# Kernel tuning notes

Measured on AMD Instinct MI355X. Metric: run time of the kernel, lower is better.

## Reference

```python
import jax, jax.numpy as jnp
import numpy as np

B, T, D = 4, 4096, 512
K = 8192  # codebook_size


def setup_inputs() -> dict:
    key = jax.random.key(0)
    k1, k2 = jax.random.split(key)
    x = jax.random.normal(k1, (B, T, D), dtype=jnp.float32)
    embed = jax.random.normal(k2, (K, D), dtype=jnp.float32)
    return {"x": x, "embed": embed}


def reference(x, embed):
    # preprocess: flatten all leading dims -> [N, D]
    shape = x.shape
    xf = x.reshape(-1, shape[-1])  # [N, D]
    # quantize: negative squared euclidean distance, argmax over codebook
    x_sq = jnp.sum(xf * xf, axis=1, keepdims=True)          # [N, 1]
    e_sq = jnp.sum(embed * embed, axis=1)[None, :]          # [1, K]
    dist = -(x_sq - 2.0 * (xf @ embed.T) + e_sq)            # [N, K]
    embed_ind = jnp.argmax(dist, axis=-1)                   # [N]
    embed_ind = embed_ind.reshape(shape[:-1])               # [B, T]
    quantize = embed[embed_ind]                             # [B, T, D]
    return (quantize, embed_ind)
```

## Files before the change

### kernel.cpp

```cpp
#include <hip/hip_runtime.h>
#include <cstddef>
#include <cstdint>

typedef unsigned short ushort_t;
typedef unsigned long long ull_t;
typedef __attribute__((ext_vector_type(8))) short short8;
typedef __attribute__((ext_vector_type(4))) float f32x4;

constexpr int D_ = 512, K_ = 8192, N_ = 16384;
constexpr float MARGIN = 0.75f;

__device__ __forceinline__ ushort_t f2bf(float f) {
  unsigned u = __float_as_uint(f);
  return (ushort_t)((u + 0x7FFFu + ((u >> 16) & 1u)) >> 16);
}
__device__ __forceinline__ unsigned flipf(float s) {
  unsigned u = __float_as_uint(s);
  return (u & 0x80000000u) ? ~u : (u | 0x80000000u);
}
__device__ __forceinline__ float unflipf(unsigned m) {
  unsigned u = (m & 0x80000000u) ? (m ^ 0x80000000u) : ~m;
  return __uint_as_float(u);
}
__device__ __forceinline__ ull_t umax64(ull_t a, ull_t b) { return a > b ? a : b; }
__device__ __forceinline__ ull_t umin64(ull_t a, ull_t b) { return a < b ? a : b; }

__device__ __forceinline__ void gld16(void* l, const void* g) {
  __builtin_amdgcn_global_load_lds((const __attribute__((address_space(1))) void*)g,
                                   (__attribute__((address_space(3))) void*)l, 16, 0, 0);
}

__global__ __launch_bounds__(256) void conv_all(const float* __restrict__ x,
                                                const float* __restrict__ e,
                                                char* __restrict__ xbt, char* __restrict__ ebt,
                                                float* __restrict__ ehs) {
  const int g = threadIdx.x & 15, rr = threadIdx.x >> 4;
  if ((int)blockIdx.x < 1024) {
    const int tile = blockIdx.x >> 3, rg = blockIdx.x & 7;
    const int r = rg * 16 + rr;
    const float4* src = (const float4*)(x + ((size_t)(tile * 128 + r)) * D_ + g * 32);
    float4 f[8];
#pragma unroll
    for (int q = 0; q < 8; ++q) f[q] = src[q];
    char* dbase = xbt + (size_t)tile * 131072 + g * 8192 + r * 16;
#pragma unroll
    for (int kq = 0; kq < 4; ++kq) {
      float4 a = f[kq * 2], b = f[kq * 2 + 1];
      short8 v;
      v[0] = (short)f2bf(a.x); v[1] = (short)f2bf(a.y); v[2] = (short)f2bf(a.z); v[3] = (short)f2bf(a.w);
      v[4] = (short)f2bf(b.x); v[5] = (short)f2bf(b.y); v[6] = (short)f2bf(b.z); v[7] = (short)f2bf(b.w);
      *(short8*)(dbase + kq * 2048) = v;
    }
  } else {
    const int bid = blockIdx.x - 1024;
    const int tile = bid >> 3, rg = bid & 7;
    const int r = rg * 16 + rr;
    const int col = tile * 128 + r;
    const float4* src = (const float4*)(e + (size_t)col * D_ + g * 32);
    float4 f[8];
    float ss = 0.f;
#pragma unroll
    for (int q = 0; q < 8; ++q) {
      f[q] = src[q];
      ss += f[q].x * f[q].x + f[q].y * f[q].y + f[q].z * f[q].z + f[q].w * f[q].w;
    }
    char* dbase = ebt + (size_t)tile * 131072 + g * 8192 + r * 16;
#pragma unroll
    for (int kq = 0; kq < 4; ++kq) {
      float4 a = f[kq * 2], b = f[kq * 2 + 1];
      short8 v;
      v[0] = (short)f2bf(a.x); v[1] = (short)f2bf(a.y); v[2] = (short)f2bf(a.z); v[3] = (short)f2bf(a.w);
      v[4] = (short)f2bf(b.x); v[5] = (short)f2bf(b.y); v[6] = (short)f2bf(b.z); v[7] = (short)f2bf(b.w);
      *(short8*)(dbase + kq * 2048) = v;
    }
#pragma unroll
    for (int m = 1; m < 16; m <<= 1) ss += __shfl_xor(ss, m);
    if (g == 0) ehs[col] = 0.5f * ss;
  }
}

__global__ __launch_bounds__(256, 4) void dist_mfma(const char* __restrict__ xbt,
                                                    const char* __restrict__ ebt,
                                                    const float* __restrict__ ehs,
                                                    ull_t* __restrict__ ppu,
                                                    float* __restrict__ pps2) {
  __shared__ alignas(16) char lds[32768];
  const int tid = threadIdx.x, w = tid >> 6, l = tid & 63;
  const int fid = blockIdx.x + blockIdx.y * 128;
  const int k8 = fid & 7, j = fid >> 3;
  const int by = k8 * 8 + (j & 7), bx = j >> 3;
  const int row0 = bx * 128, col0 = by * 128;
  const int wr = w >> 1, wc = w & 1;
  const char* xsrc = xbt + (size_t)bx * 131072;
  const char* esrc = ebt + (size_t)by * 131072;

#pragma unroll
  for (int i = 0; i < 2; ++i) {
    gld16(lds + w * 2048 + i * 1024, xsrc + w * 2048 + i * 1024 + l * 16);
    gld16(lds + 8192 + w * 2048 + i * 1024, esrc + w * 2048 + i * 1024 + l * 16);
  }
  __syncthreads();

  f32x4 acc[4][4] = {};
  for (int g = 0; g < 16; ++g) {
    char* cbase = lds + (g & 1) * 16384;
    if (g < 15) {
      char* nbase = lds + ((g + 1) & 1) * 16384;
#pragma unroll
      for (int i = 0; i < 2; ++i) {
        gld16(nbase + w * 2048 + i * 1024, xsrc + (g + 1) * 8192 + w * 2048 + i * 1024 + l * 16);
        gld16(nbase + 8192 + w * 2048 + i * 1024, esrc + (g + 1) * 8192 + w * 2048 + i * 1024 + l * 16);
      }
    }
    short8 a[4], b[4];
#pragma unroll
    for (int i = 0; i < 4; ++i)
      a[i] = *(const short8*)(cbase + (l >> 4) * 2048 + (wr * 64 + i * 16 + (l & 15)) * 16);
#pragma unroll
    for (int jj = 0; jj < 4; ++jj)
      b[jj] = *(const short8*)(cbase + 8192 + (l >> 4) * 2048 + (wc * 64 + jj * 16 + (l & 15)) * 16);
#pragma unroll
    for (int i = 0; i < 4; ++i)
#pragma unroll
      for (int jj = 0; jj < 4; ++jj)
        acc[i][jj] = __builtin_amdgcn_mfma_f32_16x16x32_bf16(a[i], b[jj], acc[i][jj], 0, 0, 0);
    __syncthreads();
  }

  float eh[4];
  unsigned ic[4];
#pragma unroll
  for (int jj = 0; jj < 4; ++jj) {
    int col = col0 + wc * 64 + jj * 16 + (l & 15);
    eh[jj] = ehs[col];
    ic[jj] = 0xFFFFFFFFu - (unsigned)col;
  }
#pragma unroll
  for (int i = 0; i < 4; ++i)
#pragma unroll
    for (int jj = 0; jj < 4; ++jj)
#pragma unroll
      for (int r = 0; r < 4; ++r)
        acc[i][jj][r] -= eh[jj];

  float mx[4][4];
#pragma unroll
  for (int i = 0; i < 4; ++i)
#pragma unroll
    for (int r = 0; r < 4; ++r)
      mx[i][r] = fmaxf(fmaxf(acc[i][0][r], acc[i][1][r]), fmaxf(acc[i][2][r], acc[i][3][r]));
#pragma unroll
  for (int m = 1; m < 16; m <<= 1)
#pragma unroll
    for (int i = 0; i < 4; ++i)
#pragma unroll
      for (int r = 0; r < 4; ++r)
        mx[i][r] = fmaxf(mx[i][r], __shfl_xor(mx[i][r], m));

  unsigned ii[4][4];
#pragma unroll
  for (int i = 0; i < 4; ++i)
#pragma unroll
    for (int r = 0; r < 4; ++r) {
      unsigned t0 = (acc[i][0][r] == mx[i][r]) ? ic[0] : 0u;
      unsigned t1 = (acc[i][1][r] == mx[i][r]) ? ic[1] : 0u;
      unsigned t2 = (acc[i][2][r] == mx[i][r]) ? ic[2] : 0u;
      unsigned t3 = (acc[i][3][r] == mx[i][r]) ? ic[3] : 0u;
      unsigned u01 = t0 > t1 ? t0 : t1, u23 = t2 > t3 ? t2 : t3;
      ii[i][r] = u01 > u23 ? u01 : u23;
    }
#pragma unroll
  for (int m = 1; m < 16; m <<= 1)
#pragma unroll
    for (int i = 0; i < 4; ++i)
#pragma unroll
      for (int r = 0; r < 4; ++r) {
        unsigned o = __shfl_xor(ii[i][r], m);
        ii[i][r] = ii[i][r] > o ? ii[i][r] : o;
      }

  float s2[4][4];
#pragma unroll
  for (int i = 0; i < 4; ++i)
#pragma unroll
    for (int r = 0; r < 4; ++r) {
      float t0 = (ic[0] == ii[i][r]) ? -3e38f : acc[i][0][r];
      float t1 = (ic[1] == ii[i][r]) ? -3e38f : acc[i][1][r];
      float t2 = (ic[2] == ii[i][r]) ? -3e38f : acc[i][2][r];
      float t3 = (ic[3] == ii[i][r]) ? -3e38f : acc[i][3][r];
      s2[i][r] = fmaxf(fmaxf(t0, t1), fmaxf(t2, t3));
    }
#pragma unroll
  for (int m = 1; m < 16; m <<= 1)
#pragma unroll
    for (int i = 0; i < 4; ++i)
#pragma unroll
      for (int r = 0; r < 4; ++r)
        s2[i][r] = fmaxf(s2[i][r], __shfl_xor(s2[i][r], m));

  const int c = l & 15, g16 = l >> 4;
  float fs1 = -3e38f, fs2 = -3e38f;
  unsigned fii = 0;
#pragma unroll
  for (int i = 0; i < 4; ++i) {
    if ((c >> 2) == i) {
      int rsel = c & 3;
      fs1 = (rsel == 0) ? mx[i][0] : (rsel == 1) ? mx[i][1] : (rsel == 2) ? mx[i][2] : mx[i][3];
      fii = (rsel == 0) ? ii[i][0] : (rsel == 1) ? ii[i][1] : (rsel == 2) ? ii[i][2] : ii[i][3];
      fs2 = (rsel == 0) ? s2[i][0] : (rsel == 1) ? s2[i][1] : (rsel == 2) ? s2[i][2] : s2[i][3];
    }
  }
  ull_t fp = ((ull_t)flipf(fs1) << 32) | fii;
  const int rib = wr * 64 + (c >> 2) * 16 + g16 * 4 + (c & 3);

  ull_t* lp = (ull_t*)lds;
  float* ls2 = (float*)(lds + 2048);
  lp[wc * 128 + rib] = fp; ls2[wc * 128 + rib] = fs2;
  __syncthreads();
  if (wc == 0) {
    ull_t op = lp[128 + rib];
    float os2 = ls2[128 + rib];
    ull_t lo = umin64(fp, op);
    fs2 = fmaxf(fmaxf(fs2, os2), unflipf((unsigned)(lo >> 32)));
    fp = umax64(fp, op);
    ppu[(size_t)(row0 + rib) * 64 + by] = fp;
    pps2[(size_t)(row0 + rib) * 64 + by] = fs2;
  }
}

__global__ __launch_bounds__(256) void finalize(const float* __restrict__ x,
                                                const float* __restrict__ embed,
                                                const float* __restrict__ ehs,
                                                const ull_t* __restrict__ ppu,
                                                const float* __restrict__ pps2,
                                                float* __restrict__ out) {
  const int row = (blockIdx.x * 256 + threadIdx.x) >> 6;
  const int l = threadIdx.x & 63;
  ull_t p = ppu[(size_t)row * 64 + l];
  float s2 = pps2[(size_t)row * 64 + l];
  ull_t gp = p;
#pragma unroll
  for (int m = 1; m < 64; m <<= 1) gp = umax64(gp, __shfl_xor(gp, m));
  float gs = unflipf((unsigned)(gp >> 32));
  float t = gs - MARGIN;
  bool cand = (unflipf((unsigned)(p >> 32)) >= t);
  bool ovf = (s2 >= t);
  ull_t b1 = __ballot(cand);
  ull_t b2 = __ballot(ovf);
  int idx;
  if (__popcll(b1) == 1 && b2 == 0ull) {
    idx = (int)(0xFFFFFFFFu - (unsigned)(gp & 0xFFFFFFFFu));
  } else {
    const float4* xr4 = (const float4*)(x + (size_t)row * D_ + l * 8);
    float4 xa = xr4[0], xc = xr4[1];
    ull_t best = 0ull;
    ull_t bb = b1;
    while (bb) {
      int b = (int)__builtin_ctzll(bb);
      bb &= bb - 1;
      ull_t pb = __shfl(p, b);
      int col = (int)(0xFFFFFFFFu - (unsigned)(pb & 0xFFFFFFFFu));
      const float4* er4 = (const float4*)(embed + (size_t)col * D_ + l * 8);
      float4 ea = er4[0], ec = er4[1];
      float s = xa.x * ea.x + xa.y * ea.y + xa.z * ea.z + xa.w * ea.w
              + xc.x * ec.x + xc.y * ec.y + xc.z * ec.z + xc.w * ec.w;
#pragma unroll
      for (int m = 1; m < 64; m <<= 1) s += __shfl_xor(s, m);
      s -= ehs[col];
      best = umax64(best, ((ull_t)flipf(s) << 32) | (0xFFFFFFFFu - (unsigned)col));
    }
    while (b2) {
      int b = (int)__builtin_ctzll(b2);
      b2 &= b2 - 1;
      int c0 = b * 128;
      const float* xr = x + (size_t)row * D_;
      const float* e0p = embed + (size_t)(c0 + l) * D_;
      const float* e1p = embed + (size_t)(c0 + 64 + l) * D_;
      float a0 = 0.f, a1 = 0.f;
      for (int d = 0; d < D_; d += 4) {
        float4 xv = *(const float4*)(xr + d);
        float4 v0 = *(const float4*)(e0p + d);
        float4 v1 = *(const float4*)(e1p + d);
        a0 = fmaf(v0.x, xv.x, fmaf(v0.y, xv.y, fmaf(v0.z, xv.z, fmaf(v0.w, xv.w, a0))));
        a1 = fmaf(v1.x, xv.x, fmaf(v1.y, xv.y, fmaf(v1.z, xv.z, fmaf(v1.w, xv.w, a1))));
      }
      float s0 = a0 - ehs[c0 + l];
      float s1 = a1 - ehs[c0 + 64 + l];
      ull_t p0 = ((ull_t)flipf(s0) << 32) | (0xFFFFFFFFu - (unsigned)(c0 + l));
      ull_t p1 = ((ull_t)flipf(s1) << 32) | (0xFFFFFFFFu - (unsigned)(c0 + 64 + l));
      ull_t pk = umax64(p0, p1);
#pragma unroll
      for (int m = 1; m < 64; m <<= 1) pk = umax64(pk, __shfl_xor(pk, m));
      best = umax64(best, pk);
    }
    idx = (int)(0xFFFFFFFFu - (unsigned)(best & 0xFFFFFFFFu));
  }
  const float4* src = (const float4*)(embed + (size_t)idx * D_);
  float4* dst = (float4*)(out + (size_t)row * D_);
  dst[l] = src[l];
  dst[l + 64] = src[l + 64];
  if (l == 0) out[(size_t)N_ * D_ + row] = (float)idx;
}

extern "C" void kernel_launch(void* const* d_in, const int* in_sizes, int n_in,
                              void* d_out, int out_size, void* d_ws, size_t ws_size,
                              hipStream_t stream) {
  const float* x = (const float*)d_in[0];
  const float* e = (const float*)d_in[1];
  float* out = (float*)d_out;

  char* ws = (char*)d_ws;
  char* xbt = ws;
  char* ebt = ws + 16777216;
  float* ehs = (float*)(ws + 25165824);
  ull_t* ppu = (ull_t*)(ws + 25198592);
  float* pps2 = (float*)(ws + 33587200);

  conv_all<<<1536, 256, 0, stream>>>(x, e, xbt, ebt, ehs);
  dist_mfma<<<dim3(128, 64), 256, 0, stream>>>(xbt, ebt, ehs, ppu, pps2);
  finalize<<<4096, 256, 0, stream>>>(x, e, ehs, ppu, pps2, out);
}
```

Before: 243.3 us.

## Load MFMA operands directly from global memory instead of LDS double-buffering

The distance GEMM kernel no longer stages x and codebook tiles through LDS with global_load_lds double buffering. Each wave now reads its bf16 fragments straight from global (L2-cached) memory, and the per-iteration __syncthreads is gone. LDS use shrinks to the small reduction buffers, which could allow higher occupancy. In exchange, fragments shared between waves are fetched redundantly from L2, and global load latency is exposed unless unrolling hides it.

```diff
diff --git a/kernel.cpp b/kernel.cpp
--- a/kernel.cpp
+++ b/kernel.cpp
@@ -24,11 +24,6 @@
 }
 __device__ __forceinline__ ull_t umax64(ull_t a, ull_t b) { return a > b ? a : b; }
 __device__ __forceinline__ ull_t umin64(ull_t a, ull_t b) { return a < b ? a : b; }
-
-__device__ __forceinline__ void gld16(void* l, const void* g) {
-  __builtin_amdgcn_global_load_lds((const __attribute__((address_space(1))) void*)g,
-                                   (__attribute__((address_space(3))) void*)l, 16, 0, 0);
-}
 
 __global__ __launch_bounds__(256) void conv_all(const float* __restrict__ x,
                                                 const float* __restrict__ e,
@@ -84,47 +79,32 @@
                                                     const float* __restrict__ ehs,
                                                     ull_t* __restrict__ ppu,
                                                     float* __restrict__ pps2) {
-  __shared__ alignas(16) char lds[32768];
+  __shared__ ull_t lp[256];
+  __shared__ float ls2[256];
   const int tid = threadIdx.x, w = tid >> 6, l = tid & 63;
   const int fid = blockIdx.x + blockIdx.y * 128;
   const int k8 = fid & 7, j = fid >> 3;
   const int by = k8 * 8 + (j & 7), bx = j >> 3;
   const int row0 = bx * 128, col0 = by * 128;
   const int wr = w >> 1, wc = w & 1;
-  const char* xsrc = xbt + (size_t)bx * 131072;
-  const char* esrc = ebt + (size_t)by * 131072;
-
-#pragma unroll
-  for (int i = 0; i < 2; ++i) {
-    gld16(lds + w * 2048 + i * 1024, xsrc + w * 2048 + i * 1024 + l * 16);
-    gld16(lds + 8192 + w * 2048 + i * 1024, esrc + w * 2048 + i * 1024 + l * 16);
-  }
-  __syncthreads();
+  const char* abase = xbt + (size_t)bx * 131072 + (l >> 4) * 2048 + wr * 1024 + (l & 15) * 16;
+  const char* bbase = ebt + (size_t)by * 131072 + (l >> 4) * 2048 + wc * 1024 + (l & 15) * 16;
 
   f32x4 acc[4][4] = {};
+#pragma unroll 4
   for (int g = 0; g < 16; ++g) {
-    char* cbase = lds + (g & 1) * 16384;
-    if (g < 15) {
-      char* nbase = lds + ((g + 1) & 1) * 16384;
-#pragma unroll
-      for (int i = 0; i < 2; ++i) {
-        gld16(nbase + w * 2048 + i * 1024, xsrc + (g + 1) * 8192 + w * 2048 + i * 1024 + l * 16);
-        gld16(nbase + 8192 + w * 2048 + i * 1024, esrc + (g + 1) * 8192 + w * 2048 + i * 1024 + l * 16);
-      }
-    }
     short8 a[4], b[4];
 #pragma unroll
     for (int i = 0; i < 4; ++i)
-      a[i] = *(const short8*)(cbase + (l >> 4) * 2048 + (wr * 64 + i * 16 + (l & 15)) * 16);
+      a[i] = *(const short8*)(abase + g * 8192 + i * 256);
 #pragma unroll
     for (int jj = 0; jj < 4; ++jj)
-      b[jj] = *(const short8*)(cbase + 8192 + (l >> 4) * 2048 + (wc * 64 + jj * 16 + (l & 15)) * 16);
+      b[jj] = *(const short8*)(bbase + g * 8192 + jj * 256);
 #pragma unroll
     for (int i = 0; i < 4; ++i)
 #pragma unroll
       for (int jj = 0; jj < 4; ++jj)
         acc[i][jj] = __builtin_amdgcn_mfma_f32_16x16x32_bf16(a[i], b[jj], acc[i][jj], 0, 0, 0);
-    __syncthreads();
   }
 
   float eh[4];
@@ -213,8 +193,6 @@
   ull_t fp = ((ull_t)flipf(fs1) << 32) | fii;
   const int rib = wr * 64 + (c >> 2) * 16 + g16 * 4 + (c & 3);
 
-  ull_t* lp = (ull_t*)lds;
-  float* ls2 = (float*)(lds + 2048);
   lp[wc * 128 + rib] = fp; ls2[wc * 128 + rib] = fs2;
   __syncthreads();
   if (wc == 0) {
```

Result: faster. 215.0 us (-11.6%).
